# Kernel tuning notes

Hardware: AMD Instinct MI355X
Metric: run time of the kernel (lower is better)

## Reference

```python
import jax, jax.numpy as jnp
import numpy as np
import math

N_HEAD = 16
K_SPARSE = 64

def setup_inputs() -> dict:
    key = jax.random.key(0)
    ks = jax.random.split(key, 12)
    B, T, C = 1, 2048, 1024
    s = 0.02
    return {
        "x":   jax.random.normal(ks[0], (B, T, C), jnp.float32),
        "Wq":  jax.random.normal(ks[1], (C, C), jnp.float32) * s,
        "bq":  jax.random.normal(ks[2], (C,), jnp.float32) * s,
        "Wk":  jax.random.normal(ks[3], (C, C), jnp.float32) * s,
        "bk":  jax.random.normal(ks[4], (C,), jnp.float32) * s,
        "Wv":  jax.random.normal(ks[5], (C, C), jnp.float32) * s,
        "bv":  jax.random.normal(ks[6], (C,), jnp.float32) * s,
        "Wo":  jax.random.normal(ks[7], (C, C), jnp.float32) * s,
        "bo":  jax.random.normal(ks[8], (C,), jnp.float32) * s,
        "Wks": jax.random.normal(ks[9], (C,), jnp.float32) * s,
        "bks": jax.random.normal(ks[10], (), jnp.float32) * s,
    }

def reference(x, Wq, bq, Wk, bk, Wv, bv, Wo, bo, Wks, bks):
    B, T, C = x.shape
    nh = N_HEAD
    hs = C // nh
    k_val = min(K_SPARSE, T)

    # projections -> (B, nh, T, hs)   (torch Linear: x @ W.T + b)
    q = (x @ Wq.T + bq).reshape(B, T, nh, hs).transpose(0, 2, 1, 3)
    k = (x @ Wk.T + bk).reshape(B, T, nh, hs).transpose(0, 2, 1, 3)
    v = (x @ Wv.T + bv).reshape(B, T, nh, hs).transpose(0, 2, 1, 3)

    # key scorer: per-token scalar score (B, T)
    key_scores = x @ Wks + bks

    # causal masking of scores, then per-query top-k key selection
    pos = jnp.arange(T)
    causal = pos[None, :] <= pos[:, None]                      # (T, T), True where key<=query
    masked = jnp.where(causal[None], key_scores[:, None, :], -jnp.inf)  # (B, T, T)
    _, top_k_idx = jax.lax.top_k(masked, k_val)                # (B, T, k)
    top_k_idx = jnp.minimum(top_k_idx, pos[None, :, None])     # clamp to <= query pos

    # gather sparse keys/values: (B, nh, T, k, hs)
    bi = jnp.arange(B)[:, None, None, None]
    hi = jnp.arange(nh)[None, :, None, None]
    gi = top_k_idx[:, None, :, :]                              # (B, 1, T, k)
    sparse_k = k[bi, hi, gi]                                   # (B, nh, T, k, hs)
    sparse_v = v[bi, hi, gi]

    scale = 1.0 / math.sqrt(hs)
    logits = jnp.einsum('bhtd,bhtkd->bhtk', q, sparse_k) * scale
    probs = jax.nn.softmax(logits, axis=-1)
    out = jnp.einsum('bhtk,bhtkd->bhtd', probs, sparse_v)      # (B, nh, T, hs)
    out = out.transpose(0, 2, 1, 3).reshape(B, T, C)
    return out @ Wo.T + bo
```

## Files before the change

kernel.cpp:

```cpp
#include <hip/hip_runtime.h>
#include <hip/hip_bf16.h>
#include <cstdint>
#include <cstddef>

#define T_DIM 2048
#define C_DIM 1024
#define NH 16
#define HS 64
#define KSP 64

#define GBM 128
#define GBN 64
#define GBK 128
#define OBM 64
#define OBN 64

typedef short short8 __attribute__((ext_vector_type(8)));
typedef float f32x4 __attribute__((ext_vector_type(4)));
typedef _Float16 half2_t __attribute__((ext_vector_type(2)));

__device__ __forceinline__ float bfu2f(unsigned short u) {
  unsigned v = ((unsigned)u) << 16;
  return __builtin_bit_cast(float, v);
}
__device__ __forceinline__ unsigned short f2bfu(float f) {
  unsigned u = __builtin_bit_cast(unsigned, f);
  unsigned r = (u + 0x7fffu + ((u >> 16) & 1u)) >> 16;
  return (unsigned short)r;
}
__device__ __forceinline__ unsigned short f2h(float f) {
  _Float16 h = (_Float16)f;
  return __builtin_bit_cast(unsigned short, h);
}
__device__ __forceinline__ float bflo(unsigned u) {
  return __builtin_bit_cast(float, u << 16);
}
__device__ __forceinline__ float bfhi(unsigned u) {
  return __builtin_bit_cast(float, u & 0xffff0000u);
}

__device__ __forceinline__ float dot2h(unsigned kbits, unsigned qbits, float acc) {
#if __has_builtin(__builtin_amdgcn_fdot2)
  return __builtin_amdgcn_fdot2(__builtin_bit_cast(half2_t, kbits),
                                __builtin_bit_cast(half2_t, qbits), acc, false);
#else
  half2_t kk = __builtin_bit_cast(half2_t, kbits);
  half2_t qq = __builtin_bit_cast(half2_t, qbits);
  return acc + (float)kk.x * (float)qq.x + (float)kk.y * (float)qq.y;
#endif
}

#define GLOAD_LDS16(gp, lp)                                                  \
  __builtin_amdgcn_global_load_lds(                                          \
      (const __attribute__((address_space(1))) void*)(gp),                   \
      (__attribute__((address_space(3))) void*)(lp), 16, 0, 0)

#define NSCORE (T_DIM / 4)
#define NCONV ((T_DIM * C_DIM + 4 * C_DIM * C_DIM) / 4 / 256)
__global__ __launch_bounds__(256) void convert_scores_kernel(
    const float* __restrict__ x, const float* __restrict__ Wq,
    const float* __restrict__ Wk, const float* __restrict__ Wv,
    const float* __restrict__ Wo, const float* __restrict__ Wks,
    const float* __restrict__ bks,
    unsigned short* __restrict__ xb, unsigned short* __restrict__ Wqb,
    unsigned short* __restrict__ Wkb, unsigned short* __restrict__ Wvb,
    unsigned short* __restrict__ Wob, float* __restrict__ scores) {
  if (blockIdx.x < NSCORE) {
    const int t = blockIdx.x * 4 + (threadIdx.x >> 6);
    const int lane = threadIdx.x & 63;
    const float* xrow = x + (size_t)t * C_DIM;
    float acc = 0.f;
    #pragma unroll 4
    for (int i = lane; i < C_DIM; i += 64)
      acc += xrow[i] * Wks[i];
    #pragma unroll
    for (int o = 32; o; o >>= 1) acc += __shfl_xor(acc, o);
    if (lane == 0) scores[t] = acc + bks[0];
    return;
  }
  const int i = (blockIdx.x - NSCORE) * 256 + threadIdx.x;
  const int NX4 = T_DIM * C_DIM / 4;
  const int NW4 = C_DIM * C_DIM / 4;
  const float* src;
  unsigned short* dst;
  int j = i;
  if (j < NX4) { src = x; dst = xb; }
  else {
    j -= NX4;
    int w = j / NW4;
    j -= w * NW4;
    src = (w == 0) ? Wq : (w == 1) ? Wk : (w == 2) ? Wv : Wo;
    dst = (w == 0) ? Wqb : (w == 1) ? Wkb : (w == 2) ? Wvb : Wob;
  }
  float4 f = reinterpret_cast<const float4*>(src)[j];
  ushort4 o;
  o.x = f2bfu(f.x); o.y = f2bfu(f.y); o.z = f2bfu(f.z); o.w = f2bfu(f.w);
  reinterpret_cast<ushort4*>(dst)[j] = o;
}

__device__ __forceinline__ void gemm_body_128x64(
    const unsigned short* __restrict__ A, const unsigned short* __restrict__ W,
    f32x4 acc[4][2], int bm, int bn, int tid,
    unsigned short* As, unsigned short* Ws) {
  const int w = tid >> 6, lane = tid & 63;
  const int quad = lane >> 4, r = lane & 15;
  const int wm = (w >> 1) * 64, wn = (w & 1) * 32;
  const int sub = lane >> 4;
  const int c = lane & 15;
  const unsigned short* Arow[8];
  const unsigned short* Wrow[4];
  #pragma unroll
  for (int i = 0; i < 8; ++i) {
    const int row = w * 32 + i * 4 + sub;
    Arow[i] = A + (size_t)(bm * GBM + row) * C_DIM + ((c ^ (row & 7)) * 8);
  }
  #pragma unroll
  for (int i = 0; i < 4; ++i) {
    const int row = w * 16 + i * 4 + sub;
    Wrow[i] = W + (size_t)(bn * GBN + row) * C_DIM + ((c ^ (row & 7)) * 8);
  }
  for (int kb = 0; kb < C_DIM; kb += GBK) {
    #pragma unroll
    for (int i = 0; i < 8; ++i)
      GLOAD_LDS16(Arow[i] + kb, &As[(w * 32 + i * 4) * GBK]);
    #pragma unroll
    for (int i = 0; i < 4; ++i)
      GLOAD_LDS16(Wrow[i] + kb, &Ws[(w * 16 + i * 4) * GBK]);
    __syncthreads();
    #pragma unroll
    for (int ks = 0; ks < 4; ++ks) {
      const int pc = ((ks * 4 + quad) ^ (r & 7)) * 8;
      short8 af[4], bfr[2];
      #pragma unroll
      for (int mi = 0; mi < 4; ++mi)
        af[mi] = *reinterpret_cast<const short8*>(&As[(wm + mi * 16 + r) * GBK + pc]);
      #pragma unroll
      for (int ni = 0; ni < 2; ++ni)
        bfr[ni] = *reinterpret_cast<const short8*>(&Ws[(wn + ni * 16 + r) * GBK + pc]);
      #pragma unroll
      for (int mi = 0; mi < 4; ++mi)
        #pragma unroll
        for (int ni = 0; ni < 2; ++ni)
          acc[mi][ni] = __builtin_amdgcn_mfma_f32_16x16x32_bf16(af[mi], bfr[ni], acc[mi][ni], 0, 0, 0);
    }
    __syncthreads();
  }
}

#define NRANK (T_DIM / 4)
__global__ __launch_bounds__(256) void gemm_qkv_rank_kernel(
    const unsigned short* __restrict__ A,
    const unsigned short* __restrict__ Wq, const unsigned short* __restrict__ Wk,
    const unsigned short* __restrict__ Wv,
    const float* __restrict__ bq, const float* __restrict__ bk,
    const float* __restrict__ bv,
    unsigned short* __restrict__ qo, unsigned short* __restrict__ ko,
    unsigned short* __restrict__ vo,
    const float* __restrict__ scores, int* __restrict__ sorted_idx) {
  __shared__ unsigned short lds[(GBM + GBN) * GBK];
  const int tid = threadIdx.x;
  if (blockIdx.x < NRANK) {
    float* ss = reinterpret_cast<float*>(lds);
    for (int j = tid; j < T_DIM; j += 256) ss[j] = scores[j];
    __syncthreads();
    const int w = tid >> 6, lane = tid & 63;
    const int i = blockIdx.x * 4 + w;
    const float si = ss[i];
    int rank = 0;
    #pragma unroll
    for (int step = 0; step < T_DIM / 64; ++step) {
      const int j = step * 64 + lane;
      const float sj = ss[j];
      rank += (int)((sj > si) || (sj == si && j < i));
    }
    #pragma unroll
    for (int o = 32; o; o >>= 1) rank += __shfl_xor(rank, o);
    if (lane == 0) sorted_idx[rank] = i;
    return;
  }
  const int bid = blockIdx.x - NRANK;
  const int per = (T_DIM / GBM) * (C_DIM / GBN);
  const int which = bid / per;
  const int rem = bid % per;
  const int bm = rem / (C_DIM / GBN);
  const int bn = rem % (C_DIM / GBN);
  const unsigned short* W = (which == 0) ? Wq : (which == 1) ? Wk : Wv;
  const float* bias = (which == 0) ? bq : (which == 1) ? bk : bv;
  unsigned short* out = (which == 0) ? qo : (which == 1) ? ko : vo;
  f32x4 acc[4][2] = {};
  gemm_body_128x64(A, W, acc, bm, bn, tid, lds, lds + GBM * GBK);
  const int w = tid >> 6, lane = tid & 63;
  const int quad = lane >> 4, r = lane & 15;
  const int wm = (w >> 1) * 64, wn = (w & 1) * 32;
  #pragma unroll
  for (int mi = 0; mi < 4; ++mi) {
    #pragma unroll
    for (int ni = 0; ni < 2; ++ni) {
      const int col = bn * GBN + wn + ni * 16 + r;
      const float bf = bias[col];
      #pragma unroll
      for (int i = 0; i < 4; ++i) {
        const int row = bm * GBM + wm + mi * 16 + quad * 4 + i;
        const float val = acc[mi][ni][i] + bf;
        out[(size_t)row * C_DIM + col] = (which == 2) ? f2bfu(val) : f2h(val);
      }
    }
  }
}

__device__ __forceinline__ void gemm_body_64x64(
    const unsigned short* __restrict__ A, const unsigned short* __restrict__ W,
    f32x4 acc[2][2], int bm, int bn, int tid) {
  __shared__ unsigned short As[OBM * GBK];
  __shared__ unsigned short Ws[OBN * GBK];
  const int w = tid >> 6, lane = tid & 63;
  const int quad = lane >> 4, r = lane & 15;
  const int wm = (w >> 1) * 32, wn = (w & 1) * 32;
  const int sub = lane >> 4;
  const int c = lane & 15;
  const unsigned short* Arow[4];
  const unsigned short* Wrow[4];
  #pragma unroll
  for (int i = 0; i < 4; ++i) {
    const int row = w * 16 + i * 4 + sub;
    Arow[i] = A + (size_t)(bm * OBM + row) * C_DIM + ((c ^ (row & 7)) * 8);
    Wrow[i] = W + (size_t)(bn * OBN + row) * C_DIM + ((c ^ (row & 7)) * 8);
  }
  for (int kb = 0; kb < C_DIM; kb += GBK) {
    #pragma unroll
    for (int i = 0; i < 4; ++i)
      GLOAD_LDS16(Arow[i] + kb, &As[(w * 16 + i * 4) * GBK]);
    #pragma unroll
    for (int i = 0; i < 4; ++i)
      GLOAD_LDS16(Wrow[i] + kb, &Ws[(w * 16 + i * 4) * GBK]);
    __syncthreads();
    #pragma unroll
    for (int ks = 0; ks < 4; ++ks) {
      const int pc = ((ks * 4 + quad) ^ (r & 7)) * 8;
      short8 af[2], bfr[2];
      #pragma unroll
      for (int mi = 0; mi < 2; ++mi)
        af[mi] = *reinterpret_cast<const short8*>(&As[(wm + mi * 16 + r) * GBK + pc]);
      #pragma unroll
      for (int ni = 0; ni < 2; ++ni)
        bfr[ni] = *reinterpret_cast<const short8*>(&Ws[(wn + ni * 16 + r) * GBK + pc]);
      #pragma unroll
      for (int mi = 0; mi < 2; ++mi)
        #pragma unroll
        for (int ni = 0; ni < 2; ++ni)
          acc[mi][ni] = __builtin_amdgcn_mfma_f32_16x16x32_bf16(af[mi], bfr[ni], acc[mi][ni], 0, 0, 0);
    }
    __syncthreads();
  }
}

__global__ __launch_bounds__(256) void gemm_o_f32_kernel(
    const unsigned short* __restrict__ A, const unsigned short* __restrict__ W,
    const float* __restrict__ bias, float* __restrict__ out) {
  const int tid = threadIdx.x;
  const int bm = blockIdx.x / (C_DIM / OBN);
  const int bn = blockIdx.x % (C_DIM / OBN);
  f32x4 acc[2][2] = {};
  gemm_body_64x64(A, W, acc, bm, bn, tid);
  const int w = tid >> 6, lane = tid & 63;
  const int quad = lane >> 4, r = lane & 15;
  const int wm = (w >> 1) * 32, wn = (w & 1) * 32;
  #pragma unroll
  for (int mi = 0; mi < 2; ++mi) {
    #pragma unroll
    for (int ni = 0; ni < 2; ++ni) {
      const int col = bn * OBN + wn + ni * 16 + r;
      const float bf = bias[col];
      #pragma unroll
      for (int i = 0; i < 4; ++i) {
        const int row = bm * OBM + wm + mi * 16 + quad * 4 + i;
        out[(size_t)row * C_DIM + col] = acc[mi][ni][i] + bf;
      }
    }
  }
}

__global__ __launch_bounds__(256) void select_kernel(
    const int* __restrict__ sorted_idx, int* __restrict__ sel) {
  const int tid = threadIdx.x;
  const int w = tid >> 6, lane = tid & 63;
  const int t = blockIdx.x * 4 + w;
  int* dst = sel + (size_t)t * KSP;
  if (t <= 63) {
    dst[lane] = ((lane < t) ? lane : t) * C_DIM;
    return;
  }
  const unsigned long long lt_mask = (1ull << lane) - 1ull;
  int count = 0;
  for (int chunk = 0; chunk < T_DIM / 64 && count < KSP; ++chunk) {
    int s = sorted_idx[chunk * 64 + lane];
    s = (s < 0) ? 0 : (s > T_DIM - 1 ? T_DIM - 1 : s);
    const bool ok = (s <= t);
    const unsigned long long mm = __ballot(ok);
    const int pos = count + __popcll(mm & lt_mask);
    if (ok && pos < KSP) dst[pos] = s * C_DIM;
    count += __popcll(mm);
  }
}

__global__ __launch_bounds__(256) void attn_kernel(
    const unsigned short* __restrict__ q, const unsigned short* __restrict__ k,
    const unsigned short* __restrict__ v, const int* __restrict__ sel,
    unsigned short* __restrict__ attn_out) {
  const int t = blockIdx.x >> 2;
  const int hg = blockIdx.x & 3;
  const int tid = threadIdx.x;
  const int w = tid >> 6, lane = tid & 63;
  const int h = hg * 4 + w;
  const int c8 = lane & 7;
  const int ksub = lane >> 3;
  const int hbase = h * HS + 8 * c8;
  const int* __restrict__ selt = sel + (size_t)t * KSP;
  uint4 qraw = *reinterpret_cast<const uint4*>(q + (size_t)t * C_DIM + hbase);
  int offr[8];
  #pragma unroll
  for (int jj = 0; jj < 8; ++jj) offr[jj] = selt[8 * jj + ksub];
  uint4 kraw[8], vraw[8];
  #pragma unroll
  for (int jj = 0; jj < 8; ++jj)
    kraw[jj] = *reinterpret_cast<const uint4*>(k + offr[jj] + hbase);
  #pragma unroll
  for (int jj = 0; jj < 8; ++jj)
    vraw[jj] = *reinterpret_cast<const uint4*>(v + offr[jj] + hbase);
  float l[8];
  #pragma unroll
  for (int jj = 0; jj < 8; ++jj) {
    const uint4 raw = kraw[jj];
    float pl = dot2h(raw.x, qraw.x, 0.f);
    pl = dot2h(raw.y, qraw.y, pl);
    pl = dot2h(raw.z, qraw.z, pl);
    pl = dot2h(raw.w, qraw.w, pl);
    pl *= 0.125f;
    pl += __shfl_xor(pl, 1);
    pl += __shfl_xor(pl, 2);
    pl += __shfl_xor(pl, 4);
    l[jj] = pl;
  }
  float m = l[0];
  #pragma unroll
  for (int jj = 1; jj < 8; ++jj) m = fmaxf(m, l[jj]);
  m = fmaxf(m, __shfl_xor(m, 8));
  m = fmaxf(m, __shfl_xor(m, 16));
  m = fmaxf(m, __shfl_xor(m, 32));
  float sum = 0.f;
  #pragma unroll
  for (int jj = 0; jj < 8; ++jj) {
    l[jj] = __expf(l[jj] - m);
    sum += l[jj];
  }
  sum += __shfl_xor(sum, 8);
  sum += __shfl_xor(sum, 16);
  sum += __shfl_xor(sum, 32);
  const float rs = 1.0f / sum;
  float a[8] = {0.f, 0.f, 0.f, 0.f, 0.f, 0.f, 0.f, 0.f};
  #pragma unroll
  for (int jj = 0; jj < 8; ++jj) {
    const uint4 raw = vraw[jj];
    const float p = l[jj] * rs;
    a[0] += p * bflo(raw.x); a[1] += p * bfhi(raw.x);
    a[2] += p * bflo(raw.y); a[3] += p * bfhi(raw.y);
    a[4] += p * bflo(raw.z); a[5] += p * bfhi(raw.z);
    a[6] += p * bflo(raw.w); a[7] += p * bfhi(raw.w);
  }
  #pragma unroll
  for (int o = 8; o <= 32; o <<= 1) {
    #pragma unroll
    for (int z = 0; z < 8; ++z) a[z] += __shfl_xor(a[z], o);
  }
  if (ksub == 0) {
    ushort4 o0, o1;
    o0.x = f2bfu(a[0]); o0.y = f2bfu(a[1]); o0.z = f2bfu(a[2]); o0.w = f2bfu(a[3]);
    o1.x = f2bfu(a[4]); o1.y = f2bfu(a[5]); o1.z = f2bfu(a[6]); o1.w = f2bfu(a[7]);
    ushort4* dst = reinterpret_cast<ushort4*>(attn_out + (size_t)t * C_DIM + hbase);
    dst[0] = o0;
    dst[1] = o1;
  }
}

extern "C" void kernel_launch(void* const* d_in, const int* in_sizes, int n_in,
                              void* d_out, int out_size, void* d_ws, size_t ws_size,
                              hipStream_t stream) {
  const float* x   = (const float*)d_in[0];
  const float* Wq  = (const float*)d_in[1];
  const float* bq  = (const float*)d_in[2];
  const float* Wk  = (const float*)d_in[3];
  const float* bk  = (const float*)d_in[4];
  const float* Wv  = (const float*)d_in[5];
  const float* bv  = (const float*)d_in[6];
  const float* Wo  = (const float*)d_in[7];
  const float* bo  = (const float*)d_in[8];
  const float* Wks = (const float*)d_in[9];
  const float* bks = (const float*)d_in[10];
  float* out = (float*)d_out;

  char* ws = (char*)d_ws;
  size_t off = 0;
  float* scores = (float*)(ws + off); off += 8192;
  int*   sorted = (int*)(ws + off);   off += 8192;
  int*   sel    = (int*)(ws + off);   off += (size_t)T_DIM * KSP * 4;
  unsigned short* xb  = (unsigned short*)(ws + off); off += (size_t)T_DIM * C_DIM * 2;
  unsigned short* Wqb = (unsigned short*)(ws + off); off += (size_t)C_DIM * C_DIM * 2;
  unsigned short* Wkb = (unsigned short*)(ws + off); off += (size_t)C_DIM * C_DIM * 2;
  unsigned short* Wvb = (unsigned short*)(ws + off); off += (size_t)C_DIM * C_DIM * 2;
  unsigned short* Wob = (unsigned short*)(ws + off); off += (size_t)C_DIM * C_DIM * 2;
  unsigned short* qb  = (unsigned short*)(ws + off); off += (size_t)T_DIM * C_DIM * 2;
  unsigned short* kb  = (unsigned short*)(ws + off); off += (size_t)T_DIM * C_DIM * 2;
  unsigned short* vb  = (unsigned short*)(ws + off); off += (size_t)T_DIM * C_DIM * 2;
  unsigned short* ab  = xb;

  convert_scores_kernel<<<NSCORE + NCONV, 256, 0, stream>>>(
      x, Wq, Wk, Wv, Wo, Wks, bks, xb, Wqb, Wkb, Wvb, Wob, scores);

  gemm_qkv_rank_kernel<<<NRANK + 3 * (T_DIM / GBM) * (C_DIM / GBN), 256, 0,
                         stream>>>(
      xb, Wqb, Wkb, Wvb, bq, bk, bv, qb, kb, vb, scores, sorted);

  select_kernel<<<T_DIM / 4, 256, 0, stream>>>(sorted, sel);

  attn_kernel<<<T_DIM * 4, 256, 0, stream>>>(qb, kb, vb, sel, ab);

  gemm_o_f32_kernel<<<(T_DIM / OBM) * (C_DIM / OBN), 256, 0, stream>>>(
      ab, Wob, bo, out);
}
```

Baseline: 162.0 us.

## Share deduplicated gathered K/V rows across 32 queries in LDS

The attention kernel now handles a block of 32 consecutive queries for one head. It builds the union of their selected key rows, deduplicates them with a shared-memory map and ballot compaction, and loads each unique K/V row into LDS once. Each query then reads K/V from LDS through a per-query slot table, so repeated global gathers of the same rows are avoided. This relies on neighbouring queries sharing most of their top-k keys, and the union is capped at 96 slots. It also adds block-wide setup work and synchronisation per block.

```diff
diff --git a/kernel.cpp b/kernel.cpp
--- a/kernel.cpp
+++ b/kernel.cpp
@@ -14,6 +14,10 @@
 #define GBK 128
 #define OBM 64
 #define OBN 64
+
+#define ATB 32
+#define USLOT 96
+#define KSTR 72
 
 typedef short short8 __attribute__((ext_vector_type(8)));
 typedef float f32x4 __attribute__((ext_vector_type(4)));
@@ -287,7 +291,7 @@
   const int t = blockIdx.x * 4 + w;
   int* dst = sel + (size_t)t * KSP;
   if (t <= 63) {
-    dst[lane] = ((lane < t) ? lane : t) * C_DIM;
+    dst[lane] = (lane < t) ? lane : t;
     return;
   }
   const unsigned long long lt_mask = (1ull << lane) - 1ull;
@@ -298,7 +302,7 @@
     const bool ok = (s <= t);
     const unsigned long long mm = __ballot(ok);
     const int pos = count + __popcll(mm & lt_mask);
-    if (ok && pos < KSP) dst[pos] = s * C_DIM;
+    if (ok && pos < KSP) dst[pos] = s;
     count += __popcll(mm);
   }
 }
@@ -307,78 +311,124 @@
     const unsigned short* __restrict__ q, const unsigned short* __restrict__ k,
     const unsigned short* __restrict__ v, const int* __restrict__ sel,
     unsigned short* __restrict__ attn_out) {
-  const int t = blockIdx.x >> 2;
-  const int hg = blockIdx.x & 3;
+  __shared__ unsigned short Kl[USLOT * KSTR];
+  __shared__ unsigned short Vl[USLOT * KSTR];
+  __shared__ short map_s[T_DIM];
+  __shared__ short slots_tab[ATB][KSP];
+  __shared__ short urows[USLOT];
+  __shared__ int Ucnt;
+  const int tb = blockIdx.x >> 4;
+  const int h = blockIdx.x & (NH - 1);
+  const int t0 = tb * ATB;
   const int tid = threadIdx.x;
   const int w = tid >> 6, lane = tid & 63;
-  const int h = hg * 4 + w;
+  #pragma unroll
+  for (int i = 0; i < T_DIM / 256; ++i) map_s[tid + i * 256] = -1;
+  __syncthreads();
+  int rowreg[ATB * KSP / 256];
+  #pragma unroll
+  for (int i = 0; i < ATB * KSP / 256; ++i) {
+    rowreg[i] = sel[(size_t)t0 * KSP + tid + i * 256];
+    map_s[rowreg[i]] = 1;
+  }
+  __syncthreads();
+  if (w == 0) {
+    const unsigned long long lt_mask = (1ull << lane) - 1ull;
+    int count = 0;
+    const int nch = (t0 + ATB + 63) >> 6;
+    for (int c = 0; c < nch; ++c) {
+      const int rowi = c * 64 + lane;
+      const bool ok = (map_s[rowi] == 1);
+      const unsigned long long mm = __ballot(ok);
+      const int pos = count + __popcll(mm & lt_mask);
+      if (ok) { map_s[rowi] = (short)pos; urows[pos] = (short)rowi; }
+      count += __popcll(mm);
+    }
+    if (lane == 0) Ucnt = count;
+  }
+  __syncthreads();
+  #pragma unroll
+  for (int i = 0; i < ATB * KSP / 256; ++i)
+    (&slots_tab[0][0])[tid + i * 256] = map_s[rowreg[i]];
+  {
+    const int U = Ucnt;
+    const int e8 = tid & 7;
+    for (int s = tid >> 3; s < U; s += 32) {
+      const int row = urows[s];
+      const size_t gb = (size_t)row * C_DIM + h * HS + e8 * 8;
+      *reinterpret_cast<uint4*>(&Kl[s * KSTR + e8 * 8]) =
+          *reinterpret_cast<const uint4*>(k + gb);
+      *reinterpret_cast<uint4*>(&Vl[s * KSTR + e8 * 8]) =
+          *reinterpret_cast<const uint4*>(v + gb);
+    }
+  }
+  __syncthreads();
   const int c8 = lane & 7;
   const int ksub = lane >> 3;
-  const int hbase = h * HS + 8 * c8;
-  const int* __restrict__ selt = sel + (size_t)t * KSP;
-  uint4 qraw = *reinterpret_cast<const uint4*>(q + (size_t)t * C_DIM + hbase);
-  int offr[8];
-  #pragma unroll
-  for (int jj = 0; jj < 8; ++jj) offr[jj] = selt[8 * jj + ksub];
-  uint4 kraw[8], vraw[8];
-  #pragma unroll
-  for (int jj = 0; jj < 8; ++jj)
-    kraw[jj] = *reinterpret_cast<const uint4*>(k + offr[jj] + hbase);
-  #pragma unroll
-  for (int jj = 0; jj < 8; ++jj)
-    vraw[jj] = *reinterpret_cast<const uint4*>(v + offr[jj] + hbase);
-  float l[8];
-  #pragma unroll
-  for (int jj = 0; jj < 8; ++jj) {
-    const uint4 raw = kraw[jj];
-    float pl = dot2h(raw.x, qraw.x, 0.f);
-    pl = dot2h(raw.y, qraw.y, pl);
-    pl = dot2h(raw.z, qraw.z, pl);
-    pl = dot2h(raw.w, qraw.w, pl);
-    pl *= 0.125f;
-    pl += __shfl_xor(pl, 1);
-    pl += __shfl_xor(pl, 2);
-    pl += __shfl_xor(pl, 4);
-    l[jj] = pl;
-  }
-  float m = l[0];
-  #pragma unroll
-  for (int jj = 1; jj < 8; ++jj) m = fmaxf(m, l[jj]);
-  m = fmaxf(m, __shfl_xor(m, 8));
-  m = fmaxf(m, __shfl_xor(m, 16));
-  m = fmaxf(m, __shfl_xor(m, 32));
-  float sum = 0.f;
-  #pragma unroll
-  for (int jj = 0; jj < 8; ++jj) {
-    l[jj] = __expf(l[jj] - m);
-    sum += l[jj];
-  }
-  sum += __shfl_xor(sum, 8);
-  sum += __shfl_xor(sum, 16);
-  sum += __shfl_xor(sum, 32);
-  const float rs = 1.0f / sum;
-  float a[8] = {0.f, 0.f, 0.f, 0.f, 0.f, 0.f, 0.f, 0.f};
-  #pragma unroll
-  for (int jj = 0; jj < 8; ++jj) {
-    const uint4 raw = vraw[jj];
-    const float p = l[jj] * rs;
-    a[0] += p * bflo(raw.x); a[1] += p * bfhi(raw.x);
-    a[2] += p * bflo(raw.y); a[3] += p * bfhi(raw.y);
-    a[4] += p * bflo(raw.z); a[5] += p * bfhi(raw.z);
-    a[6] += p * bflo(raw.w); a[7] += p * bfhi(raw.w);
-  }
-  #pragma unroll
-  for (int o = 8; o <= 32; o <<= 1) {
-    #pragma unroll
-    for (int z = 0; z < 8; ++z) a[z] += __shfl_xor(a[z], o);
-  }
-  if (ksub == 0) {
-    ushort4 o0, o1;
-    o0.x = f2bfu(a[0]); o0.y = f2bfu(a[1]); o0.z = f2bfu(a[2]); o0.w = f2bfu(a[3]);
-    o1.x = f2bfu(a[4]); o1.y = f2bfu(a[5]); o1.z = f2bfu(a[6]); o1.w = f2bfu(a[7]);
-    ushort4* dst = reinterpret_cast<ushort4*>(attn_out + (size_t)t * C_DIM + hbase);
-    dst[0] = o0;
-    dst[1] = o1;
+  for (int i = 0; i < ATB / 4; ++i) {
+    const int tt = w * (ATB / 4) + i;
+    const int t = t0 + tt;
+    const uint4 qraw =
+        *reinterpret_cast<const uint4*>(q + (size_t)t * C_DIM + h * HS + 8 * c8);
+    int slot[8];
+    #pragma unroll
+    for (int jj = 0; jj < 8; ++jj) slot[jj] = slots_tab[tt][8 * jj + ksub];
+    float l[8];
+    #pragma unroll
+    for (int jj = 0; jj < 8; ++jj) {
+      const uint4 raw =
+          *reinterpret_cast<const uint4*>(&Kl[slot[jj] * KSTR + 8 * c8]);
+      float pl = dot2h(raw.x, qraw.x, 0.f);
+      pl = dot2h(raw.y, qraw.y, pl);
+      pl = dot2h(raw.z, qraw.z, pl);
+      pl = dot2h(raw.w, qraw.w, pl);
+      pl *= 0.125f;
+      pl += __shfl_xor(pl, 1);
+      pl += __shfl_xor(pl, 2);
+      pl += __shfl_xor(pl, 4);
+      l[jj] = pl;
+    }
+    float m = l[0];
+    #pragma unroll
+    for (int jj = 1; jj < 8; ++jj) m = fmaxf(m, l[jj]);
+    m = fmaxf(m, __shfl_xor(m, 8));
+    m = fmaxf(m, __shfl_xor(m, 16));
+    m = fmaxf(m, __shfl_xor(m, 32));
+    float sum = 0.f;
+    #pragma unroll
+    for (int jj = 0; jj < 8; ++jj) {
+      l[jj] = __expf(l[jj] - m);
+      sum += l[jj];
+    }
+    sum += __shfl_xor(sum, 8);
+    sum += __shfl_xor(sum, 16);
+    sum += __shfl_xor(sum, 32);
+    const float rs = 1.0f / sum;
+    float a[8] = {0.f, 0.f, 0.f, 0.f, 0.f, 0.f, 0.f, 0.f};
+    #pragma unroll
+    for (int jj = 0; jj < 8; ++jj) {
+      const uint4 raw =
+          *reinterpret_cast<const uint4*>(&Vl[slot[jj] * KSTR + 8 * c8]);
+      const float p = l[jj] * rs;
+      a[0] += p * bflo(raw.x); a[1] += p * bfhi(raw.x);
+      a[2] += p * bflo(raw.y); a[3] += p * bfhi(raw.y);
+      a[4] += p * bflo(raw.z); a[5] += p * bfhi(raw.z);
+      a[6] += p * bflo(raw.w); a[7] += p * bfhi(raw.w);
+    }
+    #pragma unroll
+    for (int o = 8; o <= 32; o <<= 1) {
+      #pragma unroll
+      for (int z = 0; z < 8; ++z) a[z] += __shfl_xor(a[z], o);
+    }
+    if (ksub == 0) {
+      ushort4 o0, o1;
+      o0.x = f2bfu(a[0]); o0.y = f2bfu(a[1]); o0.z = f2bfu(a[2]); o0.w = f2bfu(a[3]);
+      o1.x = f2bfu(a[4]); o1.y = f2bfu(a[5]); o1.z = f2bfu(a[6]); o1.w = f2bfu(a[7]);
+      ushort4* dst =
+          reinterpret_cast<ushort4*>(attn_out + (size_t)t * C_DIM + h * HS + 8 * c8);
+      dst[0] = o0;
+      dst[1] = o1;
+    }
   }
 }
 
@@ -422,7 +472,7 @@
 
   select_kernel<<<T_DIM / 4, 256, 0, stream>>>(sorted, sel);
 
-  attn_kernel<<<T_DIM * 4, 256, 0, stream>>>(qb, kb, vb, sel, ab);
+  attn_kernel<<<(T_DIM / ATB) * NH, 256, 0, stream>>>(qb, kb, vb, sel, ab);
 
   gemm_o_f32_kernel<<<(T_DIM / OBM) * (C_DIM / OBN), 256, 0, stream>>>(
       ab, Wob, bo, out);
```

Result: slower. 170.8 us (+5.5%).
